# Kernel optimization log

Hardware: AMD Instinct MI355X
Metric: run time of the kernel (lower is better)

## Reference

```python
import jax, jax.numpy as jnp
import numpy as np

D_MODEL = 512
D_INNER = 1024   # expand * d_model
D_STATE = 16
DT_RANK = 32     # ceil(d_model / 16)
D_CONV = 4
BATCH = 4
SEQLEN = 2304
DILATIONS = (1, 2, 4)


def _dw(x, w, pad, dil=1):
    # depthwise 1D conv: x (B,C,L), w (C,1,K)
    return jax.lax.conv_general_dilated(
        x, w, window_strides=(1,), padding=[pad], rhs_dilation=(dil,),
        dimension_numbers=('NCH', 'OIH', 'NCH'), feature_group_count=x.shape[1])


def setup_inputs() -> dict:
    key = jax.random.key(0)
    ks = iter(jax.random.split(key, 32))
    nrm = lambda shape, s=0.02: jax.random.normal(next(ks), shape, jnp.float32) * s
    std = DT_RANK ** -0.5
    return dict(
        hidden_states=jax.random.normal(next(ks), (BATCH, SEQLEN, D_MODEL), jnp.float32),
        in_proj_w=nrm((5 * D_INNER, D_MODEL)),
        conv1d_w=nrm((D_INNER, 1, D_CONV), 0.2),
        conv1d_b=jnp.zeros((D_INNER,), jnp.float32),
        x_proj_w=nrm((DT_RANK + 2 * D_STATE, D_INNER)),
        dt_proj_w=jax.random.uniform(next(ks), (D_INNER, DT_RANK), jnp.float32, -std, std),
        dt_proj_b=jax.random.uniform(next(ks), (D_INNER,), jnp.float32, -5.0, -1.0),
        A_log=jnp.log(jnp.broadcast_to(jnp.arange(1, D_STATE + 1, dtype=jnp.float32), (D_INNER, D_STATE))),
        D=jnp.ones((D_INNER,), jnp.float32),
        out_proj_w=nrm((D_MODEL, 3 * D_INNER)),
        cb_local_w=nrm((D_MODEL, 1, 3), 0.2), cb_local_b=jnp.zeros((D_MODEL,), jnp.float32),
        cb_global_w=nrm((D_MODEL, 1, 1), 0.2), cb_global_b=jnp.zeros((D_MODEL,), jnp.float32),
        cb_pre_w=nrm((3, D_MODEL, 1, 1), 0.2), cb_pre_b=jnp.zeros((3, D_MODEL), jnp.float32),
        cb_dil_w=nrm((3, D_MODEL, 1, 3), 0.2), cb_dil_b=jnp.zeros((3, D_MODEL), jnp.float32),
        cb_ln_g=jnp.ones((4 * D_MODEL,), jnp.float32), cb_ln_b=jnp.zeros((4 * D_MODEL,), jnp.float32),
        cb_fuse_w=nrm((2 * D_MODEL, 4 * D_MODEL, 1)), cb_fuse_b=jnp.zeros((2 * D_MODEL,), jnp.float32),
    )


def reference(hidden_states, in_proj_w, conv1d_w, conv1d_b, x_proj_w, dt_proj_w,
              dt_proj_b, A_log, D, out_proj_w, cb_local_w, cb_local_b,
              cb_global_w, cb_global_b, cb_pre_w, cb_pre_b, cb_dil_w, cb_dil_b,
              cb_ln_g, cb_ln_b, cb_fuse_w, cb_fuse_b):
    B, L, dm = hidden_states.shape
    d_inner = D.shape[0]
    d_state = A_log.shape[1]
    dt_rank = dt_proj_w.shape[1]

    # in_proj -> (B, 5*d_inner, L)
    xz = jnp.einsum('ed,bld->bel', in_proj_w, hidden_states)
    xz_f = xz[:, :2 * d_inner]
    xz_b = xz[:, 2 * d_inner:4 * d_inner]
    xz_1 = xz[:, 4 * d_inner:]
    # bidirectional: stack forward and time-flipped backward along batch
    xzc = jnp.concatenate([xz_f, jnp.flip(xz_b, -1)], axis=0)  # (2B, 2*d_inner, L)
    x, z = xzc[:, :d_inner], xzc[:, d_inner:]

    # causal depthwise conv + SiLU
    kc = conv1d_w.shape[-1]
    x = _dw(x, conv1d_w, (kc - 1, 0)) + conv1d_b[None, :, None]
    x = jax.nn.silu(x)

    # x_proj -> dt, B, C
    x_dbl = jnp.einsum('kd,bdl->bkl', x_proj_w, x)
    dt = x_dbl[:, :dt_rank]
    Bm = x_dbl[:, dt_rank:dt_rank + d_state]
    Cm = x_dbl[:, dt_rank + d_state:]
    delta = jax.nn.softplus(jnp.einsum('dr,brl->bdl', dt_proj_w, dt) + dt_proj_b[None, :, None])
    A = -jnp.exp(A_log)  # (d, n)

    # selective scan over time
    delta_l = jnp.moveaxis(delta, 2, 0)  # (L, 2B, d)
    u_l = jnp.moveaxis(x, 2, 0)          # (L, 2B, d)
    B_l = jnp.moveaxis(Bm, 2, 0)         # (L, 2B, n)
    C_l = jnp.moveaxis(Cm, 2, 0)         # (L, 2B, n)

    def step(h, t):
        dl, ul, Bl, Cl = t
        dA = jnp.exp(dl[..., None] * A)                    # (2B, d, n)
        h = dA * h + (dl * ul)[..., None] * Bl[:, None, :]
        y = jnp.einsum('bdn,bn->bd', h, Cl)
        return h, y

    h0 = jnp.zeros((x.shape[0], d_inner, d_state), x.dtype)
    _, ys = jax.lax.scan(step, h0, (delta_l, u_l, B_l, C_l))
    y = jnp.moveaxis(ys, 0, 2)  # (2B, d, L)
    y = y + D[None, :, None] * x
    y = y * jax.nn.silu(z)
    out = jnp.concatenate([y[:B], jnp.flip(y[B:], -1)], axis=1)  # (B, 2*d_inner, L)

    # ConvBranch on xz_1 (2*dm channels -> split into xa, xc of dm each)
    xa, xc = xz_1[:, :dm], xz_1[:, dm:]
    local = jax.nn.gelu(_dw(xc, cb_local_w, (1, 1)) + cb_local_b[None, :, None], approximate=False)
    phi = jax.nn.relu(cb_global_w[:, 0, 0][None, :] * xc.mean(-1) + cb_global_b[None, :])  # (B, dm)
    feats = []
    for i, d in enumerate(DILATIONS):
        xp = cb_pre_w[i, :, 0, 0][None, :, None] * xa + cb_pre_b[i][None, :, None]
        feats.append(_dw(xp, cb_dil_w[i], (d, d), dil=d) + cb_dil_b[i][None, :, None])
    cat = jnp.concatenate(feats + [phi[:, :, None] * local], axis=1)  # (B, 4*dm, L)
    c = cat.transpose(0, 2, 1)
    mu = c.mean(-1, keepdims=True)
    var = c.var(-1, keepdims=True)
    c = (c - mu) / jnp.sqrt(var + 1e-5) * cb_ln_g + cb_ln_b
    cat = c.transpose(0, 2, 1)
    out_c = jnp.einsum('oc,bcl->bol', cb_fuse_w[:, :, 0], cat) + cb_fuse_b[None, :, None]  # (B, 2*d_inner... = d_inner? no: 2*dm, L)

    out_f = jnp.concatenate([out, out_c], axis=1)  # (B, 3*d_inner, L)
    return jnp.einsum('md,bdl->blm', out_proj_w, out_f)  # (B, L, d_model)
```

## Files before the change

### kernel.cpp

```cpp
#include <hip/hip_runtime.h>
#include <math.h>

#define L 2304
#define NB 4
#define NCH 36
#define STILE 64
#define SPAD 68
#define DLU_PAD 130

typedef __attribute__((ext_vector_type(8))) short short8v;
typedef __attribute__((ext_vector_type(4))) float f32x4;

__device__ inline unsigned short f2bf(float x) {
    unsigned u = __float_as_uint(x);
    return (unsigned short)((u + 0x7fffu + ((u >> 16) & 1u)) >> 16);
}
__device__ inline void split1(float x, unsigned short& h, unsigned short& l) {
    h = f2bf(x);
    float hf = __uint_as_float((unsigned)h << 16);
    l = f2bf(x - hf);
}

__device__ inline float row_reduce16(float v) {
    v += __int_as_float(__builtin_amdgcn_update_dpp(0, __float_as_int(v), 0xB1, 0xF, 0xF, true));
    v += __int_as_float(__builtin_amdgcn_update_dpp(0, __float_as_int(v), 0x4E, 0xF, 0xF, true));
    v += __int_as_float(__builtin_amdgcn_update_dpp(0, __float_as_int(v), 0x124, 0xF, 0xF, true));
    v += __int_as_float(__builtin_amdgcn_update_dpp(0, __float_as_int(v), 0x128, 0xF, 0xF, true));
    return v;
}

__global__ __launch_bounds__(256) void split_kernel(
    const float* __restrict__ src, unsigned short* __restrict__ hi,
    unsigned short* __restrict__ lo, int n)
{
    int i = (blockIdx.x * 256 + threadIdx.x) * 4;
    if (i >= n) return;
    float4 v = *(const float4*)(src + i);
    unsigned short h0, h1, h2, h3, l0, l1, l2, l3;
    split1(v.x, h0, l0); split1(v.y, h1, l1);
    split1(v.z, h2, l2); split1(v.w, h3, l3);
    ushort4 hv; hv.x = h0; hv.y = h1; hv.z = h2; hv.w = h3;
    ushort4 lv; lv.x = l0; lv.y = l1; lv.z = l2; lv.w = l3;
    *(ushort4*)(hi + i) = hv;
    *(ushort4*)(lo + i) = lv;
}

__global__ __launch_bounds__(256) void split_t_kernel(
    const float* __restrict__ src, unsigned short* __restrict__ hiT,
    unsigned short* __restrict__ loT, int C)
{
    __shared__ float tile[64][65];
    const int l0 = blockIdx.x * 64, c0 = blockIdx.y * 64;
    const int li = threadIdx.x & 63, q = threadIdx.x >> 6;
    for (int cc = q; cc < 64; cc += 4)
        tile[cc][li] = src[(long)(c0 + cc) * L + l0 + li];
    __syncthreads();
    const int ci = threadIdx.x & 63;
    for (int ll = q; ll < 64; ll += 4) {
        float x = tile[ci][ll];
        unsigned short h, l;
        split1(x, h, l);
        long o = (long)(l0 + ll) * C + c0 + ci;
        hiT[o] = h;
        loT[o] = l;
    }
}

__global__ __launch_bounds__(256) void gemm_mfma(
    const unsigned short* __restrict__ Ahi, const unsigned short* __restrict__ Alo, int lda,
    const unsigned short* __restrict__ Bhi, const unsigned short* __restrict__ Blo, int ldb,
    float* __restrict__ C, long cms, long cns, int K, int act,
    const float* __restrict__ emu, const float* __restrict__ ers,
    const float* __restrict__ es1, const float* __restrict__ es2)
{
    __shared__ unsigned short Ah[128 * 40], Al[128 * 40], Bh[128 * 40], Bl[128 * 40];
    const int tid = threadIdx.x;
    const int lane = tid & 63, wave = tid >> 6;
    const int wm = (wave >> 1) * 64, wn = (wave & 1) * 64;
    const int m0 = blockIdx.x * 128, n0 = blockIdx.y * 128;
    const int srow = tid >> 1, skh = (tid & 1) * 16;
    const unsigned short* gAh = Ahi + (long)(m0 + srow) * lda + skh;
    const unsigned short* gAl = Alo + (long)(m0 + srow) * lda + skh;
    const unsigned short* gBh = Bhi + (long)(n0 + srow) * ldb + skh;
    const unsigned short* gBl = Blo + (long)(n0 + srow) * ldb + skh;
    const int swoff = srow * 40 + skh;
    const int fr = lane & 15, kg = (lane >> 4) * 8;

    f32x4 acc[4][4];
#pragma unroll
    for (int i = 0; i < 4; ++i)
#pragma unroll
        for (int j = 0; j < 4; ++j) acc[i][j] = (f32x4){0.f, 0.f, 0.f, 0.f};

    for (int k0 = 0; k0 < K; k0 += 32) {
        *(uint4*)&Ah[swoff]     = *(const uint4*)(gAh + k0);
        *(uint4*)&Ah[swoff + 8] = *(const uint4*)(gAh + k0 + 8);
        *(uint4*)&Al[swoff]     = *(const uint4*)(gAl + k0);
        *(uint4*)&Al[swoff + 8] = *(const uint4*)(gAl + k0 + 8);
        *(uint4*)&Bh[swoff]     = *(const uint4*)(gBh + k0);
        *(uint4*)&Bh[swoff + 8] = *(const uint4*)(gBh + k0 + 8);
        *(uint4*)&Bl[swoff]     = *(const uint4*)(gBl + k0);
        *(uint4*)&Bl[swoff + 8] = *(const uint4*)(gBl + k0 + 8);
        __syncthreads();
        short8v bhf[4], blf[4];
#pragma unroll
        for (int nf = 0; nf < 4; ++nf) {
            bhf[nf] = *(const short8v*)&Bh[(wn + nf * 16 + fr) * 40 + kg];
            blf[nf] = *(const short8v*)&Bl[(wn + nf * 16 + fr) * 40 + kg];
        }
#pragma unroll
        for (int mf = 0; mf < 4; ++mf) {
            short8v ah = *(const short8v*)&Ah[(wm + mf * 16 + fr) * 40 + kg];
            short8v al = *(const short8v*)&Al[(wm + mf * 16 + fr) * 40 + kg];
#pragma unroll
            for (int nf = 0; nf < 4; ++nf) {
                acc[mf][nf] = __builtin_amdgcn_mfma_f32_16x16x32_bf16(ah, bhf[nf], acc[mf][nf], 0, 0, 0);
                acc[mf][nf] = __builtin_amdgcn_mfma_f32_16x16x32_bf16(ah, blf[nf], acc[mf][nf], 0, 0, 0);
                acc[mf][nf] = __builtin_amdgcn_mfma_f32_16x16x32_bf16(al, bhf[nf], acc[mf][nf], 0, 0, 0);
            }
        }
        __syncthreads();
    }
    const int rb = (lane >> 4) * 4;
#pragma unroll
    for (int mf = 0; mf < 4; ++mf) {
#pragma unroll
        for (int nf = 0; nf < 4; ++nf) {
            int n = n0 + wn + nf * 16 + fr;
            int mb = m0 + wm + mf * 16 + rb;
            if (cms == 1) {
                float4 r;
                r.x = acc[mf][nf][0]; r.y = acc[mf][nf][1];
                r.z = acc[mf][nf][2]; r.w = acc[mf][nf][3];
                *(float4*)(C + (long)n * cns + mb) = r;
            } else {
#pragma unroll
                for (int r = 0; r < 4; ++r) {
                    int m = mb + r;
                    float v = acc[mf][nf][r];
                    if (act == 2) v = (v - emu[n] * es1[m]) * ers[n] + es2[m];
                    C[(long)m * cms + n] = v;
                }
            }
        }
    }
}

__global__ __launch_bounds__(256) void gemm_mfma64(
    const unsigned short* __restrict__ Ahi, const unsigned short* __restrict__ Alo, int lda,
    const unsigned short* __restrict__ Bhi, const unsigned short* __restrict__ Blo, int ldb,
    float* __restrict__ C, long cms, long cns, int K, int act,
    const float* __restrict__ emu, const float* __restrict__ ers,
    const float* __restrict__ es1, const float* __restrict__ es2)
{
    __shared__ unsigned short Ah[64 * 40], Al[64 * 40], Bh[64 * 40], Bl[64 * 40];
    const int tid = threadIdx.x;
    const int lane = tid & 63, wave = tid >> 6;
    const int wm = (wave >> 1) * 32, wn = (wave & 1) * 32;
    const int m0 = blockIdx.x * 64, n0 = blockIdx.y * 64;
    const int srow = tid >> 2, skh = (tid & 3) * 8;
    const unsigned short* gAh = Ahi + (long)(m0 + srow) * lda + skh;
    const unsigned short* gAl = Alo + (long)(m0 + srow) * lda + skh;
    const unsigned short* gBh = Bhi + (long)(n0 + srow) * ldb + skh;
    const unsigned short* gBl = Blo + (long)(n0 + srow) * ldb + skh;
    const int swoff = srow * 40 + skh;
    const int fr = lane & 15, kg = (lane >> 4) * 8;

    f32x4 acc[2][2];
#pragma unroll
    for (int i = 0; i < 2; ++i)
#pragma unroll
        for (int j = 0; j < 2; ++j) acc[i][j] = (f32x4){0.f, 0.f, 0.f, 0.f};

    for (int k0 = 0; k0 < K; k0 += 32) {
        *(uint4*)&Ah[swoff] = *(const uint4*)(gAh + k0);
        *(uint4*)&Al[swoff] = *(const uint4*)(gAl + k0);
        *(uint4*)&Bh[swoff] = *(const uint4*)(gBh + k0);
        *(uint4*)&Bl[swoff] = *(const uint4*)(gBl + k0);
        __syncthreads();
        short8v bhf[2], blf[2];
#pragma unroll
        for (int nf = 0; nf < 2; ++nf) {
            bhf[nf] = *(const short8v*)&Bh[(wn + nf * 16 + fr) * 40 + kg];
            blf[nf] = *(const short8v*)&Bl[(wn + nf * 16 + fr) * 40 + kg];
        }
#pragma unroll
        for (int mf = 0; mf < 2; ++mf) {
            short8v ah = *(const short8v*)&Ah[(wm + mf * 16 + fr) * 40 + kg];
            short8v al = *(const short8v*)&Al[(wm + mf * 16 + fr) * 40 + kg];
#pragma unroll
            for (int nf = 0; nf < 2; ++nf) {
                acc[mf][nf] = __builtin_amdgcn_mfma_f32_16x16x32_bf16(ah, bhf[nf], acc[mf][nf], 0, 0, 0);
                acc[mf][nf] = __builtin_amdgcn_mfma_f32_16x16x32_bf16(ah, blf[nf], acc[mf][nf], 0, 0, 0);
                acc[mf][nf] = __builtin_amdgcn_mfma_f32_16x16x32_bf16(al, bhf[nf], acc[mf][nf], 0, 0, 0);
            }
        }
        __syncthreads();
    }
    const int rb = (lane >> 4) * 4;
#pragma unroll
    for (int mf = 0; mf < 2; ++mf) {
#pragma unroll
        for (int nf = 0; nf < 2; ++nf) {
            int n = n0 + wn + nf * 16 + fr;
            int mb = m0 + wm + mf * 16 + rb;
            if (cms == 1) {
                float4 r;
                r.x = acc[mf][nf][0]; r.y = acc[mf][nf][1];
                r.z = acc[mf][nf][2]; r.w = acc[mf][nf][3];
                *(float4*)(C + (long)n * cns + mb) = r;
            } else {
#pragma unroll
                for (int r = 0; r < 4; ++r) {
                    int m = mb + r;
                    float v = acc[mf][nf][r];
                    if (act == 2) v = (v - emu[n] * es1[m]) * ers[n] + es2[m];
                    C[(long)m * cms + n] = v;
                }
            }
        }
    }
}

__global__ __launch_bounds__(256) void gemm_f32(
    const float* __restrict__ A, int lda,
    const float* __restrict__ B, long ldb, int b_nk, long bbs,
    float* __restrict__ C, long cms, long cns, long cbs,
    int M, int N, int K,
    const float* __restrict__ bias, int act,
    const float* __restrict__ emu, const float* __restrict__ ers,
    const float* __restrict__ es1, const float* __restrict__ es2)
{
    __shared__ float As[16][65];
    __shared__ float Bs[16][65];
    const int tid = threadIdx.x;
    const int tx = tid & 15, ty = tid >> 4;
    const int m0 = blockIdx.x * 64, n0 = blockIdx.y * 64;
    const int bz = blockIdx.z;
    const float* Bb = B + (long)bz * bbs;
    float acc[4][4];
#pragma unroll
    for (int i = 0; i < 4; ++i)
#pragma unroll
        for (int j = 0; j < 4; ++j) acc[i][j] = 0.f;

    for (int k0 = 0; k0 < K; k0 += 16) {
        {
            int m = tid >> 2, kq = (tid & 3) << 2;
            float4 v = *(const float4*)(A + (long)(m0 + m) * lda + (k0 + kq));
            As[kq + 0][m] = v.x; As[kq + 1][m] = v.y; As[kq + 2][m] = v.z; As[kq + 3][m] = v.w;
        }
        if (b_nk) {
            int n = tid >> 2, kq = (tid & 3) << 2;
            float4 v = *(const float4*)(Bb + (long)(n0 + n) * ldb + (k0 + kq));
            Bs[kq + 0][n] = v.x; Bs[kq + 1][n] = v.y; Bs[kq + 2][n] = v.z; Bs[kq + 3][n] = v.w;
        } else {
            int k = tid >> 4, nq = (tid & 15) << 2;
            float4 v = *(const float4*)(Bb + (long)(k0 + k) * ldb + (n0 + nq));
            Bs[k][nq + 0] = v.x; Bs[k][nq + 1] = v.y; Bs[k][nq + 2] = v.z; Bs[k][nq + 3] = v.w;
        }
        __syncthreads();
#pragma unroll
        for (int kk = 0; kk < 16; ++kk) {
            float a[4], b[4];
#pragma unroll
            for (int i = 0; i < 4; ++i) a[i] = As[kk][ty * 4 + i];
#pragma unroll
            for (int j = 0; j < 4; ++j) b[j] = Bs[kk][tx * 4 + j];
#pragma unroll
            for (int i = 0; i < 4; ++i)
#pragma unroll
                for (int j = 0; j < 4; ++j) acc[i][j] = fmaf(a[i], b[j], acc[i][j]);
        }
        __syncthreads();
    }
#pragma unroll
    for (int i = 0; i < 4; ++i) {
        int m = m0 + ty * 4 + i;
        float bs = bias ? bias[m] : 0.f;
        float s1 = es1 ? es1[m] : 0.f;
        float s2 = es2 ? es2[m] : 0.f;
#pragma unroll
        for (int j = 0; j < 4; ++j) {
            int n = n0 + tx * 4 + j;
            float v = acc[i][j] + bs;
            if (act == 1) v = (v > 20.f) ? v : log1pf(expf(v));
            else if (act == 2) {
                float mu = emu[n];
                float rs = ers[n];
                v = (v - mu * s1) * rs + s2;
            }
            C[(long)bz * cbs + (long)m * cms + (long)n * cns] = v;
        }
    }
}

__global__ __launch_bounds__(256) void xproj_partial(
    const float* __restrict__ W, const float* __restrict__ xconv,
    float* __restrict__ P)
{
    __shared__ float As[16][65];
    __shared__ float Bs[16][65];
    const int tid = threadIdx.x;
    const int tx = tid & 15, ty = tid >> 4;
    const int n0 = blockIdx.x * 64;
    const int dir = blockIdx.y, sl = blockIdx.z;
    const float* A = W + sl * 256;
    const float* B = xconv + ((long)dir * 1024 + sl * 256) * L;
    float* Pp = P + ((long)sl * 2 + dir) * 64 * L;
    float acc[4][4];
#pragma unroll
    for (int i = 0; i < 4; ++i)
#pragma unroll
        for (int j = 0; j < 4; ++j) acc[i][j] = 0.f;

    for (int k0 = 0; k0 < 256; k0 += 16) {
        {
            int m = tid >> 2, kq = (tid & 3) << 2;
            float4 v = *(const float4*)(A + (long)m * 1024 + (k0 + kq));
            As[kq + 0][m] = v.x; As[kq + 1][m] = v.y; As[kq + 2][m] = v.z; As[kq + 3][m] = v.w;
        }
        {
            int k = tid >> 4, nq = (tid & 15) << 2;
            float4 v = *(const float4*)(B + (long)(k0 + k) * L + (n0 + nq));
            Bs[k][nq + 0] = v.x; Bs[k][nq + 1] = v.y; Bs[k][nq + 2] = v.z; Bs[k][nq + 3] = v.w;
        }
        __syncthreads();
#pragma unroll
        for (int kk = 0; kk < 16; ++kk) {
            float a[4], b[4];
#pragma unroll
            for (int i = 0; i < 4; ++i) a[i] = As[kk][ty * 4 + i];
#pragma unroll
            for (int j = 0; j < 4; ++j) b[j] = Bs[kk][tx * 4 + j];
#pragma unroll
            for (int i = 0; i < 4; ++i)
#pragma unroll
                for (int j = 0; j < 4; ++j) acc[i][j] = fmaf(a[i], b[j], acc[i][j]);
        }
        __syncthreads();
    }
#pragma unroll
    for (int i = 0; i < 4; ++i) {
        int m = ty * 4 + i;
        float4 r;
        r.x = acc[i][0]; r.y = acc[i][1]; r.z = acc[i][2]; r.w = acc[i][3];
        *(float4*)(Pp + (long)m * L + n0 + tx * 4) = r;
    }
}

__global__ __launch_bounds__(256) void xproj_reduce(
    const float* __restrict__ P, float* __restrict__ xdbl)
{
    const long E = (long)2 * 64 * L;
    long i = ((long)blockIdx.x * 256 + threadIdx.x) * 4;
    float4 a = *(const float4*)(P + i);
    float4 b = *(const float4*)(P + E + i);
    float4 c = *(const float4*)(P + 2 * E + i);
    float4 d = *(const float4*)(P + 3 * E + i);
    float4 r;
    r.x = (a.x + b.x) + (c.x + d.x);
    r.y = (a.y + b.y) + (c.y + d.y);
    r.z = (a.z + b.z) + (c.z + d.z);
    r.w = (a.w + b.w) + (c.w + d.w);
    *(float4*)(xdbl + i) = r;
}

__global__ __launch_bounds__(256) void mamba_conv_kernel(
    const float* __restrict__ xz_b, const float* __restrict__ w,
    const float* __restrict__ bias, float* __restrict__ xout)
{
    long idx = (long)blockIdx.x * 256 + threadIdx.x;
    int l = (int)(idx % L);
    long r = idx / L;
    int d = (int)(r % 1024);
    int dir = (int)(r / 1024);
    const float* src = xz_b + ((dir ? 2048 : 0) + (long)d) * L;
    float acc = bias[d];
#pragma unroll
    for (int j = 0; j < 4; ++j) {
        int t = l - 3 + j;
        if (t >= 0) {
            float v = dir ? src[L - 1 - t] : src[t];
            acc = fmaf(w[d * 4 + j], v, acc);
        }
    }
    xout[idx] = acc / (1.f + expf(-acc));
}

__global__ __launch_bounds__(256) void scan_pass1(
    const float* __restrict__ delta_b, const float* __restrict__ xconv_b,
    const float* __restrict__ xdbl_b, const float* __restrict__ A_log,
    float* __restrict__ hend, float* __restrict__ pAb)
{
    __shared__ float s_dlu[16][DLU_PAD];
    __shared__ float s_B[16][SPAD];
    const int tid = threadIdx.x;
    const int dir = blockIdx.y, ch = blockIdx.z;
    const int n = tid & 15, dloc = tid >> 4;
    const int d0 = blockIdx.x * 16;
    const int d = d0 + dloc;
    const int t0 = ch * STILE;
    const float Adn = -expf(A_log[d * 16 + n]);
    const float* dl_p = delta_b + ((long)dir * 1024 + d0) * L;
    const float* u_p  = xconv_b + ((long)dir * 1024 + d0) * L;
    const float* B_p  = xdbl_b + ((long)dir * 64 + 32) * L;
    const int lch = tid >> 4, lq = tid & 15;
    {
        float4 a = *(const float4*)(dl_p + (long)lch * L + t0 + lq * 4);
        float4 b = *(const float4*)(u_p + (long)lch * L + t0 + lq * 4);
        float4 w0; w0.x = a.x; w0.y = b.x; w0.z = a.y; w0.w = b.y;
        float4 w1; w1.x = a.z; w1.y = b.z; w1.z = a.w; w1.w = b.w;
        *(float4*)&s_dlu[lch][lq * 8] = w0;
        *(float4*)&s_dlu[lch][lq * 8 + 4] = w1;
        float4 v = *(const float4*)(B_p + (long)lch * L + t0 + lq * 4);
        *(float4*)&s_B[lch][lq * 4] = v;
    }
    __syncthreads();
    float h = 0.f, p = 1.f;
#pragma unroll 4
    for (int tt = 0; tt < STILE; ++tt) {
        float2 dlu = *(const float2*)&s_dlu[dloc][tt * 2];
        float Bv = s_B[n][tt];
        float dA = __expf(dlu.x * Adn);
        h = fmaf(dA, h, dlu.x * dlu.y * Bv);
        p *= dA;
    }
    long sidx = (((long)dir * NCH + ch) * 1024 + d) * 16 + n;
    hend[sidx] = h;
    pAb[sidx] = p;
}

__global__ __launch_bounds__(256) void scan_fix(
    const float* __restrict__ hend, const float* __restrict__ pAb,
    float* __restrict__ hin)
{
    int tid = blockIdx.x * 256 + threadIdx.x;
    int dir = tid >> 14;
    int rest = tid & 16383;
    float h = 0.f;
#pragma unroll
    for (int c = 0; c < NCH; ++c) {
        long idx = (((long)dir * NCH + c) << 14) + rest;
        hin[idx] = h;
        h = hend[idx] + pAb[idx] * h;
    }
}

__global__ __launch_bounds__(256) void scan_pass2(
    const float* __restrict__ delta_b, const float* __restrict__ xconv_b,
    const float* __restrict__ xdbl_b, const float* __restrict__ xz_b,
    const float* __restrict__ A_log, const float* __restrict__ Dvec,
    const float* __restrict__ hin, float* __restrict__ out_fb)
{
    __shared__ float s_dlu[16][DLU_PAD];
    __shared__ float s_BC[16][DLU_PAD];
    const int tid = threadIdx.x;
    const int dir = blockIdx.y, ch = blockIdx.z;
    const int n = tid & 15, dloc = tid >> 4;
    const int d0 = blockIdx.x * 16;
    const int d = d0 + dloc;
    const int t0 = ch * STILE;
    const int opos0 = dir ? (L - STILE - t0) : t0;
    const float Adn = -expf(A_log[d * 16 + n]);
    const float Dd = Dvec[d];
    const float* dl_p = delta_b + ((long)dir * 1024 + d0) * L;
    const float* u_p  = xconv_b + ((long)dir * 1024 + d0) * L;
    const float* B_p  = xdbl_b + ((long)dir * 64 + 32) * L;
    const float* C_p  = xdbl_b + ((long)dir * 64 + 48) * L;
    const float* z_p  = xz_b + ((dir ? 3072 : 1024) + (long)d0) * L;
    float* o_p = out_fb + ((dir ? 1024 : 0) + (long)d0) * L;
    const int lch = tid >> 4, lq = tid & 15;
    {
        float4 a = *(const float4*)(dl_p + (long)lch * L + t0 + lq * 4);
        float4 b = *(const float4*)(u_p + (long)lch * L + t0 + lq * 4);
        float4 w0; w0.x = a.x; w0.y = b.x; w0.z = a.y; w0.w = b.y;
        float4 w1; w1.x = a.z; w1.y = b.z; w1.z = a.w; w1.w = b.w;
        *(float4*)&s_dlu[lch][lq * 8] = w0;
        *(float4*)&s_dlu[lch][lq * 8 + 4] = w1;
        float4 c = *(const float4*)(B_p + (long)lch * L + t0 + lq * 4);
        float4 e = *(const float4*)(C_p + (long)lch * L + t0 + lq * 4);
        float4 x0; x0.x = c.x; x0.y = e.x; x0.z = c.y; x0.w = e.y;
        float4 x1; x1.x = c.z; x1.y = e.z; x1.z = c.w; x1.w = e.w;
        *(float4*)&s_BC[lch][lq * 8] = x0;
        *(float4*)&s_BC[lch][lq * 8 + 4] = x1;
    }
    __syncthreads();
    float h = hin[(((long)dir * NCH + ch) * 1024 + d) * 16 + n];
#pragma unroll 4
    for (int tt = 0; tt < STILE; ++tt) {
        float2 dlu = *(const float2*)&s_dlu[dloc][tt * 2];
        float2 bc = *(const float2*)&s_BC[n][tt * 2];
        float dA = __expf(dlu.x * Adn);
        h = fmaf(dA, h, dlu.x * dlu.y * bc.x);
        float y = row_reduce16(h * bc.y);
        if (n == 0) s_dlu[dloc][tt * 2] = y + Dd * dlu.y;
    }
    {
        float* po = o_p + (long)lch * L + opos0;
        const float* pz = z_p + (long)lch * L + opos0;
        int oo = lq * 4;
        float4 zv = *(const float4*)(pz + oo);
        float y0 = s_dlu[lch][(dir ? 63 - oo : oo) * 2];
        float y1 = s_dlu[lch][(dir ? 62 - oo : oo + 1) * 2];
        float y2 = s_dlu[lch][(dir ? 61 - oo : oo + 2) * 2];
        float y3 = s_dlu[lch][(dir ? 60 - oo : oo + 3) * 2];
        float4 r;
        r.x = y0 * (zv.x / (1.f + __expf(-zv.x)));
        r.y = y1 * (zv.y / (1.f + __expf(-zv.y)));
        r.z = y2 * (zv.z / (1.f + __expf(-zv.z)));
        r.w = y3 * (zv.w / (1.f + __expf(-zv.w)));
        *(float4*)(po + oo) = r;
    }
}

__global__ __launch_bounds__(256) void mean_phi_kernel(
    const float* __restrict__ xz_b, const float* __restrict__ gw,
    const float* __restrict__ gb, float* __restrict__ phi_b)
{
    int c = blockIdx.x;
    const float* src = xz_b + (4608 + (long)c) * L;
    float s = 0.f;
    for (int l = threadIdx.x; l < L; l += 256) s += src[l];
    __shared__ float red[256];
    red[threadIdx.x] = s;
    __syncthreads();
    for (int st = 128; st > 0; st >>= 1) {
        if (threadIdx.x < st) red[threadIdx.x] += red[threadIdx.x + st];
        __syncthreads();
    }
    if (threadIdx.x == 0) {
        float m = red[0] / (float)L;
        phi_b[c] = fmaxf(gw[c] * m + gb[c], 0.f);
    }
}

__global__ __launch_bounds__(256) void cat_build_kernel(
    const float* __restrict__ xz_b,
    const float* __restrict__ lw, const float* __restrict__ lb,
    const float* __restrict__ pw, const float* __restrict__ pb,
    const float* __restrict__ dw, const float* __restrict__ db,
    const float* __restrict__ phi_b, float* __restrict__ cat_b)
{
    long idx = (long)blockIdx.x * 256 + threadIdx.x;
    int l = (int)(idx % L);
    int cc = (int)(idx / L);
    float val;
    if (cc < 1536) {
        int i = cc >> 9, c = cc & 511, dil = 1 << i;
        const float* xa = xz_b + (4096 + (long)c) * L;
        float pwv = pw[i * 512 + c], pbv = pb[i * 512 + c];
        const float* w = dw + ((long)i * 512 + c) * 3;
        float acc = db[i * 512 + c];
#pragma unroll
        for (int k = 0; k < 3; ++k) {
            int t = l + (k - 1) * dil;
            if (t >= 0 && t < L) acc += (pwv * xa[t] + pbv) * w[k];
        }
        val = acc;
    } else {
        int c = cc & 511;
        const float* xc = xz_b + (4608 + (long)c) * L;
        float acc = lb[c];
#pragma unroll
        for (int k = 0; k < 3; ++k) {
            int t = l - 1 + k;
            if (t >= 0 && t < L) acc += xc[t] * lw[c * 3 + k];
        }
        float g = 0.5f * acc * (1.f + erff(acc * 0.70710678118f));
        val = phi_b[c] * g;
    }
    cat_b[idx] = val;
}

__global__ __launch_bounds__(256) void ln_partial_kernel(
    const float* __restrict__ cat_b, float* __restrict__ ps, float* __restrict__ pq)
{
    int l = blockIdx.x * 256 + threadIdx.x;
    int g = blockIdx.y;
    const float* p = cat_b + (long)g * 64 * L + l;
    float s = 0.f, q = 0.f;
#pragma unroll 8
    for (int c = 0; c < 64; ++c) {
        float v = p[(long)c * L];
        s += v;
        q = fmaf(v, v, q);
    }
    ps[g * L + l] = s;
    pq[g * L + l] = q;
}

__global__ __launch_bounds__(256) void ln_final_kernel(
    const float* __restrict__ ps, const float* __restrict__ pq,
    float* __restrict__ mu_b, float* __restrict__ rsig_b)
{
    int l = blockIdx.x * 256 + threadIdx.x;
    float s = 0.f, q = 0.f;
#pragma unroll
    for (int g = 0; g < 32; ++g) {
        s += ps[g * L + l];
        q += pq[g * L + l];
    }
    float m = s * (1.f / 2048.f);
    float var = q * (1.f / 2048.f) - m * m;
    mu_b[l] = m;
    rsig_b[l] = rsqrtf(var + 1e-5f);
}

__global__ __launch_bounds__(256) void ln_stats_kernel(
    const float* __restrict__ cat_b, float* __restrict__ mu_b, float* __restrict__ rsig_b)
{
    int tx = threadIdx.x & 63, ty = threadIdx.x >> 6;
    int l = blockIdx.x * 64 + tx;
    float s = 0.f, s2 = 0.f;
    for (int c = ty; c < 2048; c += 4) {
        float v = cat_b[(long)c * L + l];
        s += v;
        s2 += v * v;
    }
    __shared__ float rs[4][64], rq[4][64];
    rs[ty][tx] = s;
    rq[ty][tx] = s2;
    __syncthreads();
    if (ty == 0) {
        float S = rs[0][tx] + rs[1][tx] + rs[2][tx] + rs[3][tx];
        float Q = rq[0][tx] + rq[1][tx] + rq[2][tx] + rq[3][tx];
        float m = S * (1.f / 2048.f);
        float var = Q * (1.f / 2048.f) - m * m;
        mu_b[l] = m;
        rsig_b[l] = rsqrtf(var + 1e-5f);
    }
}

__global__ __launch_bounds__(256) void fuse_pre_kernel(
    const float* __restrict__ fw, const float* __restrict__ g,
    const float* __restrict__ lbn, const float* __restrict__ fb,
    float* __restrict__ wg, float* __restrict__ S1, float* __restrict__ S2)
{
    int o = blockIdx.x;
    float s1 = 0.f, s2 = 0.f;
    for (int c = threadIdx.x; c < 2048; c += 256) {
        float w = fw[(long)o * 2048 + c];
        float v = w * g[c];
        wg[(long)o * 2048 + c] = v;
        s1 += v;
        s2 += w * lbn[c];
    }
    __shared__ float r1[256], r2[256];
    r1[threadIdx.x] = s1;
    r2[threadIdx.x] = s2;
    __syncthreads();
    for (int st = 128; st > 0; st >>= 1) {
        if (threadIdx.x < st) {
            r1[threadIdx.x] += r1[threadIdx.x + st];
            r2[threadIdx.x] += r2[threadIdx.x + st];
        }
        __syncthreads();
    }
    if (threadIdx.x == 0) {
        S1[o] = r1[0];
        S2[o] = r2[0] + fb[o];
    }
}

__global__ __launch_bounds__(256) void fuse_pre_split_kernel(
    const float* __restrict__ fw, const float* __restrict__ g,
    const float* __restrict__ lbn, const float* __restrict__ fb,
    unsigned short* __restrict__ wg_hi, unsigned short* __restrict__ wg_lo,
    float* __restrict__ S1, float* __restrict__ S2)
{
    int o = blockIdx.x;
    float s1 = 0.f, s2 = 0.f;
    for (int c = threadIdx.x; c < 2048; c += 256) {
        float w = fw[(long)o * 2048 + c];
        float v = w * g[c];
        unsigned short h, l;
        split1(v, h, l);
        wg_hi[(long)o * 2048 + c] = h;
        wg_lo[(long)o * 2048 + c] = l;
        s1 += v;
        s2 += w * lbn[c];
    }
    __shared__ float r1[256], r2[256];
    r1[threadIdx.x] = s1;
    r2[threadIdx.x] = s2;
    __syncthreads();
    for (int st = 128; st > 0; st >>= 1) {
        if (threadIdx.x < st) {
            r1[threadIdx.x] += r1[threadIdx.x + st];
            r2[threadIdx.x] += r2[threadIdx.x + st];
        }
        __syncthreads();
    }
    if (threadIdx.x == 0) {
        S1[o] = r1[0];
        S2[o] = r2[0] + fb[o];
    }
}

extern "C" void kernel_launch(void* const* d_in, const int* in_sizes, int n_in,
                              void* d_out, int out_size, void* d_ws, size_t ws_size,
                              hipStream_t stream)
{
    const float* hidden     = (const float*)d_in[0];
    const float* in_proj_w  = (const float*)d_in[1];
    const float* conv1d_w   = (const float*)d_in[2];
    const float* conv1d_b   = (const float*)d_in[3];
    const float* x_proj_w   = (const float*)d_in[4];
    const float* dt_proj_w  = (const float*)d_in[5];
    const float* dt_proj_b  = (const float*)d_in[6];
    const float* A_log      = (const float*)d_in[7];
    const float* Dvec       = (const float*)d_in[8];
    const float* out_proj_w = (const float*)d_in[9];
    const float* cb_local_w = (const float*)d_in[10];
    const float* cb_local_b = (const float*)d_in[11];
    const float* cb_global_w= (const float*)d_in[12];
    const float* cb_global_b= (const float*)d_in[13];
    const float* cb_pre_w   = (const float*)d_in[14];
    const float* cb_pre_b   = (const float*)d_in[15];
    const float* cb_dil_w   = (const float*)d_in[16];
    const float* cb_dil_b   = (const float*)d_in[17];
    const float* cb_ln_g    = (const float*)d_in[18];
    const float* cb_ln_b    = (const float*)d_in[19];
    const float* cb_fuse_w  = (const float*)d_in[20];
    const float* cb_fuse_b  = (const float*)d_in[21];

    float* ws = (float*)d_ws;
    const size_t CSZ = (size_t)2 * NCH * 1024 * 16;

    size_t off = 0;
    float* S1    = ws + off; off += 1024;
    float* S2    = ws + off; off += 1024;
    float* xz_b  = ws + off; off += (size_t)5120 * L;
    float* out_fb= ws + off; off += (size_t)3072 * L;
    float* cat_b = ws + off; off += (size_t)2048 * L;
    float* delta_b = cat_b;
    float* xconv_b = ws + off; off += (size_t)2048 * L;
    float* xdbl_b  = ws + off; off += (size_t)128 * L;
    float* mu_b    = ws + off; off += L;
    float* rsig_b  = ws + off; off += L;
    float* phi_b   = ws + off; off += 512;
    float* lnps    = ws + off; off += (size_t)32 * L;
    float* lnpq    = ws + off; off += (size_t)32 * L;
    float* hend = ws + off; off += CSZ;
    float* pAb  = ws + off; off += CSZ;
    float* hin  = ws + off; off += CSZ;
    unsigned short* wg_hi  = (unsigned short*)(ws + off); off += (size_t)1024 * 2048 / 2;
    unsigned short* wg_lo  = (unsigned short*)(ws + off); off += (size_t)1024 * 2048 / 2;
    unsigned short* inW_hi = (unsigned short*)(ws + off); off += (size_t)5120 * 512 / 2;
    unsigned short* inW_lo = (unsigned short*)(ws + off); off += (size_t)5120 * 512 / 2;
    unsigned short* outW_hi= (unsigned short*)(ws + off); off += (size_t)512 * 3072 / 2;
    unsigned short* outW_lo= (unsigned short*)(ws + off); off += (size_t)512 * 3072 / 2;
    unsigned short* BT_hi  = (unsigned short*)(ws + off); off += (size_t)3072 * L / 2;
    unsigned short* BT_lo  = (unsigned short*)(ws + off); off += (size_t)3072 * L / 2;
    size_t need_mfma = off * sizeof(float);

    float* xpP = out_fb;

    if (ws_size >= need_mfma) {
        fuse_pre_split_kernel<<<1024, 256, 0, stream>>>(
            cb_fuse_w, cb_ln_g, cb_ln_b, cb_fuse_b, wg_hi, wg_lo, S1, S2);
        split_kernel<<<(5120 * 512) / 1024, 256, 0, stream>>>(in_proj_w, inW_hi, inW_lo, 5120 * 512);
        split_kernel<<<(512 * 3072) / 1024, 256, 0, stream>>>(out_proj_w, outW_hi, outW_lo, 512 * 3072);

        for (int b = 0; b < NB; ++b) {
            const float* hid_b = hidden + (size_t)b * L * 512;
            float* out_b = (float*)d_out + (size_t)b * L * 512;

            split_kernel<<<(L * 512) / 1024, 256, 0, stream>>>(hid_b, BT_hi, BT_lo, L * 512);
            gemm_mfma<<<dim3(5120 / 128, L / 128), 256, 0, stream>>>(
                inW_hi, inW_lo, 512, BT_hi, BT_lo, 512,
                xz_b, L, 1, 512, 0, nullptr, nullptr, nullptr, nullptr);

            mean_phi_kernel<<<512, 256, 0, stream>>>(xz_b, cb_global_w, cb_global_b, phi_b);
            cat_build_kernel<<<(2048 * L) / 256, 256, 0, stream>>>(
                xz_b, cb_local_w, cb_local_b, cb_pre_w, cb_pre_b, cb_dil_w, cb_dil_b, phi_b, cat_b);
            ln_partial_kernel<<<dim3(L / 256, 32), 256, 0, stream>>>(cat_b, lnps, lnpq);
            ln_final_kernel<<<L / 256, 256, 0, stream>>>(lnps, lnpq, mu_b, rsig_b);
            split_t_kernel<<<dim3(L / 64, 2048 / 64), 256, 0, stream>>>(cat_b, BT_hi, BT_lo, 2048);
            gemm_mfma64<<<dim3(1024 / 64, L / 64), 256, 0, stream>>>(
                wg_hi, wg_lo, 2048, BT_hi, BT_lo, 2048,
                out_fb + (long)2048 * L, L, 1, 2048, 2, mu_b, rsig_b, S1, S2);

            mamba_conv_kernel<<<(2 * 1024 * L) / 256, 256, 0, stream>>>(
                xz_b, conv1d_w, conv1d_b, xconv_b);
            xproj_partial<<<dim3(L / 64, 2, 4), 256, 0, stream>>>(
                x_proj_w, xconv_b, xpP);
            xproj_reduce<<<(2 * 64 * L / 4) / 256, 256, 0, stream>>>(xpP, xdbl_b);
            gemm_f32<<<dim3(1024 / 64, L / 64, 2), 256, 0, stream>>>(
                dt_proj_w, 32, xdbl_b, L, 0, (long)64 * L,
                delta_b, L, 1, (long)1024 * L, 1024, L, 32,
                dt_proj_b, 1, nullptr, nullptr, nullptr, nullptr);
            scan_pass1<<<dim3(64, 2, NCH), 256, 0, stream>>>(
                delta_b, xconv_b, xdbl_b, A_log, hend, pAb);
            scan_fix<<<128, 256, 0, stream>>>(hend, pAb, hin);
            scan_pass2<<<dim3(64, 2, NCH), 256, 0, stream>>>(
                delta_b, xconv_b, xdbl_b, xz_b, A_log, Dvec, hin, out_fb);

            split_t_kernel<<<dim3(L / 64, 3072 / 64), 256, 0, stream>>>(out_fb, BT_hi, BT_lo, 3072);
            gemm_mfma64<<<dim3(512 / 64, L / 64), 256, 0, stream>>>(
                outW_hi, outW_lo, 3072, BT_hi, BT_lo, 3072,
                out_b, 1, 512, 3072, 0, nullptr, nullptr, nullptr, nullptr);
        }
        return;
    }

    off = 0;
    float* wg    = ws + off; off += (size_t)1024 * 2048;
    S1    = ws + off; off += 1024;
    S2    = ws + off; off += 1024;
    xz_b  = ws + off; off += (size_t)5120 * L;
    out_fb= ws + off; off += (size_t)3072 * L;
    cat_b = ws + off; off += (size_t)2048 * L;
    delta_b = cat_b;
    xconv_b = ws + off; off += (size_t)2048 * L;
    xdbl_b  = ws + off; off += (size_t)128 * L;
    mu_b    = ws + off; off += L;
    rsig_b  = ws + off; off += L;
    phi_b   = ws + off; off += 512;
    hend = ws + off; off += CSZ;
    pAb  = ws + off; off += CSZ;
    hin  = ws + off; off += CSZ;
    if (ws_size < off * sizeof(float)) return;

    fuse_pre_kernel<<<1024, 256, 0, stream>>>(cb_fuse_w, cb_ln_g, cb_ln_b, cb_fuse_b, wg, S1, S2);

    for (int b = 0; b < NB; ++b) {
        const float* hid_b = hidden + (size_t)b * L * 512;
        float* out_b = (float*)d_out + (size_t)b * L * 512;

        gemm_f32<<<dim3(5120 / 64, L / 64, 1), 256, 0, stream>>>(
            in_proj_w, 512, hid_b, 512, 1, 0,
            xz_b, L, 1, 0, 5120, L, 512,
            nullptr, 0, nullptr, nullptr, nullptr, nullptr);

        mean_phi_kernel<<<512, 256, 0, stream>>>(xz_b, cb_global_w, cb_global_b, phi_b);
        cat_build_kernel<<<(2048 * L) / 256, 256, 0, stream>>>(
            xz_b, cb_local_w, cb_local_b, cb_pre_w, cb_pre_b, cb_dil_w, cb_dil_b, phi_b, cat_b);
        ln_stats_kernel<<<L / 64, 256, 0, stream>>>(cat_b, mu_b, rsig_b);
        gemm_f32<<<dim3(1024 / 64, L / 64, 1), 256, 0, stream>>>(
            wg, 2048, cat_b, L, 0, 0,
            out_fb + (long)2048 * L, L, 1, 0, 1024, L, 2048,
            nullptr, 2, mu_b, rsig_b, S1, S2);

        mamba_conv_kernel<<<(2 * 1024 * L) / 256, 256, 0, stream>>>(
            xz_b, conv1d_w, conv1d_b, xconv_b);
        gemm_f32<<<dim3(1, L / 64, 2), 256, 0, stream>>>(
            x_proj_w, 1024, xconv_b, L, 0, (long)1024 * L,
            xdbl_b, L, 1, (long)64 * L, 64, L, 1024,
            nullptr, 0, nullptr, nullptr, nullptr, nullptr);
        gemm_f32<<<dim3(1024 / 64, L / 64, 2), 256, 0, stream>>>(
            dt_proj_w, 32, xdbl_b, L, 0, (long)64 * L,
            delta_b, L, 1, (long)1024 * L, 1024, L, 32,
            dt_proj_b, 1, nullptr, nullptr, nullptr, nullptr);
        scan_pass1<<<dim3(64, 2, NCH), 256, 0, stream>>>(
            delta_b, xconv_b, xdbl_b, A_log, hend, pAb);
        scan_fix<<<128, 256, 0, stream>>>(hend, pAb, hin);
        scan_pass2<<<dim3(64, 2, NCH), 256, 0, stream>>>(
            delta_b, xconv_b, xdbl_b, xz_b, A_log, Dvec, hin, out_fb);

        gemm_f32<<<dim3(512 / 64, L / 64, 1), 256, 0, stream>>>(
            out_proj_w, 3072, out_fb, L, 0, 0,
            out_b, 1, 512, 0, 512, L, 3072,
            nullptr, 0, nullptr, nullptr, nullptr, nullptr);
    }
}
```

Baseline: 1.492 ms.

## Use 128x64 split-K MFMA tiles for fuse and out-proj GEMMs with reduce kernels

```diff
diff --git a/kernel.cpp b/kernel.cpp
--- a/kernel.cpp
+++ b/kernel.cpp
@@ -146,37 +146,41 @@
     }
 }
 
-__global__ __launch_bounds__(256) void gemm_mfma64(
+__global__ __launch_bounds__(256) void gemm_mfma128x64sk(
     const unsigned short* __restrict__ Ahi, const unsigned short* __restrict__ Alo, int lda,
     const unsigned short* __restrict__ Bhi, const unsigned short* __restrict__ Blo, int ldb,
-    float* __restrict__ C, long cms, long cns, int K, int act,
-    const float* __restrict__ emu, const float* __restrict__ ers,
-    const float* __restrict__ es1, const float* __restrict__ es2)
-{
-    __shared__ unsigned short Ah[64 * 40], Al[64 * 40], Bh[64 * 40], Bl[64 * 40];
+    float* __restrict__ P, int KS, int Mstride)
+{
+    __shared__ unsigned short Ah[128 * 40], Al[128 * 40], Bh[64 * 40], Bl[64 * 40];
     const int tid = threadIdx.x;
     const int lane = tid & 63, wave = tid >> 6;
-    const int wm = (wave >> 1) * 32, wn = (wave & 1) * 32;
-    const int m0 = blockIdx.x * 64, n0 = blockIdx.y * 64;
-    const int srow = tid >> 2, skh = (tid & 3) * 8;
-    const unsigned short* gAh = Ahi + (long)(m0 + srow) * lda + skh;
-    const unsigned short* gAl = Alo + (long)(m0 + srow) * lda + skh;
-    const unsigned short* gBh = Bhi + (long)(n0 + srow) * ldb + skh;
-    const unsigned short* gBl = Blo + (long)(n0 + srow) * ldb + skh;
-    const int swoff = srow * 40 + skh;
+    const int wm = (wave >> 1) * 64, wn = (wave & 1) * 32;
+    const int m0 = blockIdx.x * 128, n0 = blockIdx.y * 64;
+    const int sl = blockIdx.z;
+    const int kbase = sl * KS;
+    const int srowA = tid >> 1, skhA = (tid & 1) * 16;
+    const unsigned short* gAh = Ahi + (long)(m0 + srowA) * lda + kbase + skhA;
+    const unsigned short* gAl = Alo + (long)(m0 + srowA) * lda + kbase + skhA;
+    const int swoffA = srowA * 40 + skhA;
+    const int srowB = tid >> 2, skhB = (tid & 3) * 8;
+    const unsigned short* gBh = Bhi + (long)(n0 + srowB) * ldb + kbase + skhB;
+    const unsigned short* gBl = Blo + (long)(n0 + srowB) * ldb + kbase + skhB;
+    const int swoffB = srowB * 40 + skhB;
     const int fr = lane & 15, kg = (lane >> 4) * 8;
 
-    f32x4 acc[2][2];
-#pragma unroll
-    for (int i = 0; i < 2; ++i)
+    f32x4 acc[4][2];
+#pragma unroll
+    for (int i = 0; i < 4; ++i)
 #pragma unroll
         for (int j = 0; j < 2; ++j) acc[i][j] = (f32x4){0.f, 0.f, 0.f, 0.f};
 
-    for (int k0 = 0; k0 < K; k0 += 32) {
-        *(uint4*)&Ah[swoff] = *(const uint4*)(gAh + k0);
-        *(uint4*)&Al[swoff] = *(const uint4*)(gAl + k0);
-        *(uint4*)&Bh[swoff] = *(const uint4*)(gBh + k0);
-        *(uint4*)&Bl[swoff] = *(const uint4*)(gBl + k0);
+    for (int k0 = 0; k0 < KS; k0 += 32) {
+        *(uint4*)&Ah[swoffA]     = *(const uint4*)(gAh + k0);
+        *(uint4*)&Ah[swoffA + 8] = *(const uint4*)(gAh + k0 + 8);
+        *(uint4*)&Al[swoffA]     = *(const uint4*)(gAl + k0);
+        *(uint4*)&Al[swoffA + 8] = *(const uint4*)(gAl + k0 + 8);
+        *(uint4*)&Bh[swoffB]     = *(const uint4*)(gBh + k0);
+        *(uint4*)&Bl[swoffB]     = *(const uint4*)(gBl + k0);
         __syncthreads();
         short8v bhf[2], blf[2];
 #pragma unroll
@@ -185,7 +189,7 @@
             blf[nf] = *(const short8v*)&Bl[(wn + nf * 16 + fr) * 40 + kg];
         }
 #pragma unroll
-        for (int mf = 0; mf < 2; ++mf) {
+        for (int mf = 0; mf < 4; ++mf) {
             short8v ah = *(const short8v*)&Ah[(wm + mf * 16 + fr) * 40 + kg];
             short8v al = *(const short8v*)&Al[(wm + mf * 16 + fr) * 40 + kg];
 #pragma unroll
@@ -198,27 +202,58 @@
         __syncthreads();
     }
     const int rb = (lane >> 4) * 4;
-#pragma unroll
-    for (int mf = 0; mf < 2; ++mf) {
+    float* Pp = P + (long)sl * Mstride * L;
+#pragma unroll
+    for (int mf = 0; mf < 4; ++mf) {
 #pragma unroll
         for (int nf = 0; nf < 2; ++nf) {
             int n = n0 + wn + nf * 16 + fr;
             int mb = m0 + wm + mf * 16 + rb;
-            if (cms == 1) {
-                float4 r;
-                r.x = acc[mf][nf][0]; r.y = acc[mf][nf][1];
-                r.z = acc[mf][nf][2]; r.w = acc[mf][nf][3];
-                *(float4*)(C + (long)n * cns + mb) = r;
-            } else {
-#pragma unroll
-                for (int r = 0; r < 4; ++r) {
-                    int m = mb + r;
-                    float v = acc[mf][nf][r];
-                    if (act == 2) v = (v - emu[n] * es1[m]) * ers[n] + es2[m];
-                    C[(long)m * cms + n] = v;
-                }
-            }
-        }
+            float4 r;
+            r.x = acc[mf][nf][0]; r.y = acc[mf][nf][1];
+            r.z = acc[mf][nf][2]; r.w = acc[mf][nf][3];
+            *(float4*)(Pp + (long)n * Mstride + mb) = r;
+        }
+    }
+}
+
+__global__ __launch_bounds__(256) void out_reduce(
+    const float* __restrict__ P, float* __restrict__ out)
+{
+    const long E = (long)512 * L;
+    long i = ((long)blockIdx.x * 256 + threadIdx.x) * 4;
+    float4 a = *(const float4*)(P + i);
+    float4 b = *(const float4*)(P + E + i);
+    float4 c = *(const float4*)(P + 2 * E + i);
+    float4 d = *(const float4*)(P + 3 * E + i);
+    float4 r;
+    r.x = (a.x + b.x) + (c.x + d.x);
+    r.y = (a.y + b.y) + (c.y + d.y);
+    r.z = (a.z + b.z) + (c.z + d.z);
+    r.w = (a.w + b.w) + (c.w + d.w);
+    *(float4*)(out + i) = r;
+}
+
+__global__ __launch_bounds__(256) void fuse_reduce(
+    const float* __restrict__ P,
+    const float* __restrict__ emu, const float* __restrict__ ers,
+    const float* __restrict__ es1, const float* __restrict__ es2,
+    float* __restrict__ out)
+{
+    __shared__ float tile[64][65];
+    const int m0 = blockIdx.x * 64, n0 = blockIdx.y * 64;
+    const int li = threadIdx.x & 63, q = threadIdx.x >> 6;
+    const long E = (long)1024 * L;
+    for (int nn = q; nn < 64; nn += 4) {
+        long base = (long)(n0 + nn) * 1024 + m0 + li;
+        tile[nn][li] = P[base] + P[E + base];
+    }
+    __syncthreads();
+    for (int mm = q; mm < 64; mm += 4) {
+        int m = m0 + mm, n = n0 + li;
+        float v = tile[li][mm];
+        v = (v - emu[n] * es1[m]) * ers[n] + es2[m];
+        out[(long)m * L + n] = v;
     }
 }
 
@@ -756,6 +791,8 @@
     size_t need_mfma = off * sizeof(float);
 
     float* xpP = out_fb;
+    float* fsP = cat_b;
+    float* opP = cat_b;
 
     if (ws_size >= need_mfma) {
         fuse_pre_split_kernel<<<1024, 256, 0, stream>>>(
@@ -778,9 +815,10 @@
             ln_partial_kernel<<<dim3(L / 256, 32), 256, 0, stream>>>(cat_b, lnps, lnpq);
             ln_final_kernel<<<L / 256, 256, 0, stream>>>(lnps, lnpq, mu_b, rsig_b);
             split_t_kernel<<<dim3(L / 64, 2048 / 64), 256, 0, stream>>>(cat_b, BT_hi, BT_lo, 2048);
-            gemm_mfma64<<<dim3(1024 / 64, L / 64), 256, 0, stream>>>(
-                wg_hi, wg_lo, 2048, BT_hi, BT_lo, 2048,
-                out_fb + (long)2048 * L, L, 1, 2048, 2, mu_b, rsig_b, S1, S2);
+            gemm_mfma128x64sk<<<dim3(1024 / 128, L / 64, 2), 256, 0, stream>>>(
+                wg_hi, wg_lo, 2048, BT_hi, BT_lo, 2048, fsP, 1024, 1024);
+            fuse_reduce<<<dim3(1024 / 64, L / 64), 256, 0, stream>>>(
+                fsP, mu_b, rsig_b, S1, S2, out_fb + (long)2048 * L);
 
             mamba_conv_kernel<<<(2 * 1024 * L) / 256, 256, 0, stream>>>(
                 xz_b, conv1d_w, conv1d_b, xconv_b);
@@ -798,9 +836,9 @@
                 delta_b, xconv_b, xdbl_b, xz_b, A_log, Dvec, hin, out_fb);
 
             split_t_kernel<<<dim3(L / 64, 3072 / 64), 256, 0, stream>>>(out_fb, BT_hi, BT_lo, 3072);
-            gemm_mfma64<<<dim3(512 / 64, L / 64), 256, 0, stream>>>(
-                outW_hi, outW_lo, 3072, BT_hi, BT_lo, 3072,
-                out_b, 1, 512, 3072, 0, nullptr, nullptr, nullptr, nullptr);
+            gemm_mfma128x64sk<<<dim3(512 / 128, L / 64, 4), 256, 0, stream>>>(
+                outW_hi, outW_lo, 3072, BT_hi, BT_lo, 3072, opP, 768, 512);
+            out_reduce<<<(512 * L / 4) / 256, 256, 0, stream>>>(opP, out_b);
         }
         return;
     }
```

New measurement: 1.399 ms. 1.07x faster.
